# Kernel optimization log

Measured on AMD Instinct MI355X. Metric: run time of the kernel, lower is better.

## Reference

```python
import jax, jax.numpy as jnp
import numpy as np

DIM = 1024
NUM_HEADS = 16
HEAD_DIM = DIM // NUM_HEADS


def setup_inputs() -> dict:
    key = jax.random.key(0)
    k1, k2, k3, k4, k5 = jax.random.split(key, 5)
    scale = 0.02
    return {
        "x": jax.random.normal(k1, (4, 2048, DIM), dtype=jnp.float32),
        "w_qkv": jax.random.normal(k2, (DIM, 3 * DIM), dtype=jnp.float32) * scale,
        "b_qkv": jax.random.normal(k3, (3 * DIM,), dtype=jnp.float32) * scale,
        "w_proj": jax.random.normal(k4, (DIM, DIM), dtype=jnp.float32) * scale,
        "b_proj": jax.random.normal(k5, (DIM,), dtype=jnp.float32) * scale,
    }


def reference(x, w_qkv, b_qkv, w_proj, b_proj):
    B, N, C = x.shape
    H, D = NUM_HEADS, HEAD_DIM
    qkv = x @ w_qkv + b_qkv                      # [B, N, 3C]
    qkv = qkv.reshape(B, N, 3, H, D)
    q = qkv[:, :, 0].transpose(0, 2, 1, 3)       # [B, H, N, D]
    k = qkv[:, :, 1].transpose(0, 2, 1, 3)
    v = qkv[:, :, 2].transpose(0, 2, 1, 3)
    attn = jnp.einsum("bhnd,bhmd->bhnm", q, k) / (D ** 0.5)  # [B, H, N, N]
    attn = jax.nn.softmax(attn, axis=-1)
    out = jnp.einsum("bhnm,bhmd->bhnd", attn, v)  # [B, H, N, D]
    out = out.transpose(0, 2, 1, 3).reshape(B, N, C)
    return out @ w_proj + b_proj
```

## Files before the change

### kernel.cpp

```cpp
#include <hip/hip_runtime.h>
#include <stdint.h>

typedef __bf16 bf16_t;
typedef __bf16 bf16x8 __attribute__((ext_vector_type(8)));
typedef __bf16 bf16x4 __attribute__((ext_vector_type(4)));
typedef float  f32x4  __attribute__((ext_vector_type(4)));

__device__ __forceinline__ void g2l16(const void* g, void* l) {
    __builtin_amdgcn_global_load_lds(
        (const __attribute__((address_space(1))) unsigned int*)g,
        (__attribute__((address_space(3))) unsigned int*)l, 16, 0, 0);
}


__global__ __launch_bounds__(256) void cvt_bf16_kernel(
    const float* __restrict__ in, bf16_t* __restrict__ out, int n)
{
    int i = blockIdx.x * 256 + threadIdx.x;
    int idx = i * 4;
    if (idx >= n) return;
    const float4 v = *(const float4*)(in + idx);
    bf16x4 o;
    o[0] = (bf16_t)v.x; o[1] = (bf16_t)v.y; o[2] = (bf16_t)v.z; o[3] = (bf16_t)v.w;
    *(bf16x4*)(out + idx) = o;
}

__global__ __launch_bounds__(256) void tcvt_kernel(
    const float* __restrict__ in, bf16_t* __restrict__ out, int R, int C)
{
    __shared__ float t[32][33];
    const int c0 = blockIdx.x * 32, r0 = blockIdx.y * 32;
    const int x = threadIdx.x & 31, y = threadIdx.x >> 5;
    #pragma unroll
    for (int i = 0; i < 32; i += 8)
        t[y + i][x] = in[(size_t)(r0 + y + i) * C + c0 + x];
    __syncthreads();
    #pragma unroll
    for (int i = 0; i < 32; i += 8)
        out[(size_t)(c0 + y + i) * R + r0 + x] = (bf16_t)t[x][y + i];
}

__device__ __forceinline__ void gemm128(
    const bf16_t* __restrict__ A, const bf16_t* __restrict__ Bt, const int K,
    bf16_t* sA, bf16_t* sB, const int m0, const int n0, f32x4 acc[4][4])
{
    const int tid  = threadIdx.x;
    const int lane = tid & 63;
    const int w    = tid >> 6;
    const int wm   = (w >> 1) * 64;
    const int wn   = (w & 1) * 64;
    const int col0 = lane & 15;
    const int quad = lane >> 4;

    #pragma unroll
    for (int mt = 0; mt < 4; ++mt)
        #pragma unroll
        for (int nt = 0; nt < 4; ++nt)
            acc[mt][nt] = (f32x4){0.f, 0.f, 0.f, 0.f};

    const int srow = tid >> 3;
    const int jsw  = ((tid & 7) ^ (srow & 7)) << 3;
    const bf16_t* Ab = A  + (size_t)(m0 + srow) * K + jsw;
    const bf16_t* Bb = Bt + (size_t)(n0 + srow) * K + jsw;

    for (int kb = 0; kb < K; kb += 64) {
        #pragma unroll
        for (int it = 0; it < 4; ++it) {
            g2l16(Ab + (size_t)(it * 32) * K + kb, sA + (size_t)(it * 256 + tid) * 8);
            g2l16(Bb + (size_t)(it * 32) * K + kb, sB + (size_t)(it * 256 + tid) * 8);
        }
        __syncthreads();
        #pragma unroll
        for (int ks = 0; ks < 2; ++ks) {
            const int jg = ks * 4 + quad;
            bf16x8 af[4], bv[4];
            #pragma unroll
            for (int mt = 0; mt < 4; ++mt) {
                const int ra = wm + mt * 16 + col0;
                af[mt] = *(const bf16x8*)(sA + ra * 64 + ((jg ^ (ra & 7)) << 3));
            }
            #pragma unroll
            for (int nt = 0; nt < 4; ++nt) {
                const int rb = wn + nt * 16 + col0;
                bv[nt] = *(const bf16x8*)(sB + rb * 64 + ((jg ^ (rb & 7)) << 3));
            }
            #pragma unroll
            for (int mt = 0; mt < 4; ++mt)
                #pragma unroll
                for (int nt = 0; nt < 4; ++nt)
                    acc[mt][nt] = __builtin_amdgcn_mfma_f32_16x16x32_bf16(
                        af[mt], bv[nt], acc[mt][nt], 0, 0, 0);
        }
        __syncthreads();
    }
}

#define QSCALE 0.18033688f
__global__ __launch_bounds__(256) void qkv_gemm_kernel(
    const bf16_t* __restrict__ x, const bf16_t* __restrict__ wT,
    const float* __restrict__ bias,
    bf16_t* __restrict__ q, bf16_t* __restrict__ k, bf16_t* __restrict__ vT)
{
    __shared__ bf16_t sA[128 * 64];
    __shared__ bf16_t sB[128 * 64];
    const int m0 = blockIdx.y * 128;
    const int n0 = blockIdx.x * 128;
    f32x4 acc[4][4];
    gemm128(x, wT, 1024, sA, sB, m0, n0, acc);

    const int tid = threadIdx.x, lane = tid & 63, w = tid >> 6;
    const int wm = (w >> 1) * 64, wn = (w & 1) * 64;
    const int col0 = lane & 15, quad = lane >> 4;
    const int sel = n0 >> 10;

    #pragma unroll
    for (int mt = 0; mt < 4; ++mt) {
        const int m_base = m0 + wm + mt * 16 + quad * 4;
        const int b = m_base >> 11;
        const int t = m_base & 2047;
        #pragma unroll
        for (int nt = 0; nt < 4; ++nt) {
            const int n = n0 + wn + nt * 16 + col0;
            const float bvv = bias[n];
            const int h = (n >> 6) & 15, d = n & 63;
            const size_t bh = (size_t)b * 16 + h;
            if (sel == 0) {
                #pragma unroll
                for (int r = 0; r < 4; ++r)
                    q[(bh * 2048 + t + r) * 64 + d] = (bf16_t)((acc[mt][nt][r] + bvv) * QSCALE);
            } else if (sel == 1) {
                #pragma unroll
                for (int r = 0; r < 4; ++r)
                    k[(bh * 2048 + t + r) * 64 + d] = (bf16_t)(acc[mt][nt][r] + bvv);
            } else {
                #pragma unroll
                for (int r = 0; r < 4; ++r)
                    vT[(bh * 64 + d) * 2048 + t + r] = (bf16_t)(acc[mt][nt][r] + bvv);
            }
        }
    }
}

__global__ __launch_bounds__(256) void proj_gemm_kernel(
    const bf16_t* __restrict__ a, const bf16_t* __restrict__ wT,
    const float* __restrict__ bias, float* __restrict__ out)
{
    __shared__ bf16_t sA[128 * 64];
    __shared__ bf16_t sB[128 * 64];
    const int m0 = blockIdx.y * 128;
    const int n0 = blockIdx.x * 128;
    f32x4 acc[4][4];
    gemm128(a, wT, 1024, sA, sB, m0, n0, acc);

    const int tid = threadIdx.x, lane = tid & 63, w = tid >> 6;
    const int wm = (w >> 1) * 64, wn = (w & 1) * 64;
    const int col0 = lane & 15, quad = lane >> 4;
    #pragma unroll
    for (int mt = 0; mt < 4; ++mt) {
        const int m_base = m0 + wm + mt * 16 + quad * 4;
        #pragma unroll
        for (int nt = 0; nt < 4; ++nt) {
            const int n = n0 + wn + nt * 16 + col0;
            const float bvv = bias[n];
            #pragma unroll
            for (int r = 0; r < 4; ++r)
                out[(size_t)(m_base + r) * 1024 + n] = acc[mt][nt][r] + bvv;
        }
    }
}

#define SP_STRIDE 72
__global__ __launch_bounds__(256) void attn_kernel(
    const bf16_t* __restrict__ q, const bf16_t* __restrict__ k,
    const bf16_t* __restrict__ vT, bf16_t* __restrict__ out)
{
    __shared__ __align__(16) char smem[18432 + 16384 + 16384];
    bf16_t* sQ = (bf16_t*)smem;
    bf16_t* sP = (bf16_t*)smem;
    bf16_t* sK = (bf16_t*)(smem + 18432);
    bf16_t* sV = (bf16_t*)(smem + 18432 + 16384);

    const int bh = blockIdx.y;
    const int qb = blockIdx.x;
    const int tid = threadIdx.x, lane = tid & 63, w = tid >> 6;
    const int col0 = lane & 15, quad = lane >> 4;

    const bf16_t* qbase = q  + ((size_t)bh * 2048 + qb * 128) * 64;
    const bf16_t* kbase = k  + (size_t)bh * 2048 * 64;
    const bf16_t* vbase = vT + (size_t)bh * 64 * 2048;

    const int srow8  = tid >> 3;
    const int jsw8   = ((tid & 7) ^ (srow8 & 7)) << 3;
    const int srow16 = tid >> 4;
    const int jsw16  = ((tid & 15) ^ (srow16 & 15)) << 3;

    #pragma unroll
    for (int it = 0; it < 4; ++it)
        g2l16(qbase + (size_t)(it * 32 + srow8) * 64 + jsw8,
              sQ + (size_t)(it * 256 + tid) * 8);
    __syncthreads();

    bf16x8 qf[2][2];
    #pragma unroll
    for (int mt = 0; mt < 2; ++mt)
        #pragma unroll
        for (int ks = 0; ks < 2; ++ks) {
            const int rq = w * 32 + mt * 16 + col0;
            const int jg = ks * 4 + quad;
            qf[mt][ks] = *(const bf16x8*)(sQ + rq * 64 + ((jg ^ (rq & 7)) << 3));
        }

    f32x4 oacc[2][4];
    float row_l[2][4];
    #pragma unroll
    for (int mt = 0; mt < 2; ++mt) {
        #pragma unroll
        for (int nt = 0; nt < 4; ++nt) oacc[mt][nt] = (f32x4){0.f, 0.f, 0.f, 0.f};
        #pragma unroll
        for (int r = 0; r < 4; ++r) row_l[mt][r] = 0.f;
    }

    for (int kv = 0; kv < 16; ++kv) {
        __syncthreads();
        const bf16_t* kg = kbase + (size_t)kv * 128 * 64;
        #pragma unroll
        for (int it = 0; it < 4; ++it)
            g2l16(kg + (size_t)(it * 32 + srow8) * 64 + jsw8,
                  sK + (size_t)(it * 256 + tid) * 8);
        #pragma unroll
        for (int it = 0; it < 4; ++it) {
            const int d = it * 16 + srow16;
            g2l16(vbase + (size_t)d * 2048 + kv * 128 + jsw16,
                  sV + (size_t)(it * 256 + tid) * 8);
        }
        __syncthreads();

        f32x4 s[2][8];
        #pragma unroll
        for (int mt = 0; mt < 2; ++mt)
            #pragma unroll
            for (int nt = 0; nt < 8; ++nt) s[mt][nt] = (f32x4){0.f, 0.f, 0.f, 0.f};
        #pragma unroll
        for (int ks = 0; ks < 2; ++ks) {
            const int jg = ks * 4 + quad;
            bf16x8 kf[8];
            #pragma unroll
            for (int nt = 0; nt < 8; ++nt) {
                const int rk = nt * 16 + col0;
                kf[nt] = *(const bf16x8*)(sK + rk * 64 + ((jg ^ (rk & 7)) << 3));
            }
            #pragma unroll
            for (int mt = 0; mt < 2; ++mt)
                #pragma unroll
                for (int nt = 0; nt < 8; ++nt)
                    s[mt][nt] = __builtin_amdgcn_mfma_f32_16x16x32_bf16(
                        qf[mt][ks], kf[nt], s[mt][nt], 0, 0, 0);
        }

        #pragma unroll
        for (int mt = 0; mt < 2; ++mt)
            #pragma unroll
            for (int r = 0; r < 4; ++r) {
                float rs = 0.f;
                #pragma unroll
                for (int nt = 0; nt < 8; ++nt) {
                    const float p = __builtin_amdgcn_exp2f(s[mt][nt][r]);
                    s[mt][nt][r] = p;
                    rs += p;
                }
                row_l[mt][r] += rs;
            }

        #pragma unroll
        for (int half = 0; half < 2; ++half) {
            #pragma unroll
            for (int mt = 0; mt < 2; ++mt)
                #pragma unroll
                for (int nt = 0; nt < 4; ++nt)
                    #pragma unroll
                    for (int r = 0; r < 4; ++r)
                        sP[(w * 32 + mt * 16 + quad * 4 + r) * SP_STRIDE + nt * 16 + col0] =
                            (bf16_t)s[mt][half * 4 + nt][r];
            #pragma unroll
            for (int ks = 0; ks < 2; ++ks) {
                bf16x8 pf[2], vf[4];
                #pragma unroll
                for (int mt = 0; mt < 2; ++mt)
                    pf[mt] = *(const bf16x8*)(sP + (w * 32 + mt * 16 + col0) * SP_STRIDE
                                              + ks * 32 + quad * 8);
                #pragma unroll
                for (int nt = 0; nt < 4; ++nt) {
                    const int dv = nt * 16 + col0;
                    const int jg = half * 8 + ks * 4 + quad;
                    vf[nt] = *(const bf16x8*)(sV + dv * 128 + ((jg ^ (dv & 15)) << 3));
                }
                #pragma unroll
                for (int mt = 0; mt < 2; ++mt)
                    #pragma unroll
                    for (int nt = 0; nt < 4; ++nt)
                        oacc[mt][nt] = __builtin_amdgcn_mfma_f32_16x16x32_bf16(
                            pf[mt], vf[nt], oacc[mt][nt], 0, 0, 0);
            }
        }
    }

    const int b = bh >> 4, h = bh & 15;
    #pragma unroll
    for (int mt = 0; mt < 2; ++mt) {
        #pragma unroll
        for (int r = 0; r < 4; ++r) {
            float l = row_l[mt][r];
            #pragma unroll
            for (int off = 1; off < 16; off <<= 1) l += __shfl_xor(l, off);
            const float inv = 1.0f / l;
            const int t = qb * 128 + w * 32 + mt * 16 + quad * 4 + r;
            const size_t rowbase = ((size_t)b * 2048 + t) * 1024 + h * 64;
            #pragma unroll
            for (int nt = 0; nt < 4; ++nt)
                out[rowbase + nt * 16 + col0] = (bf16_t)(oacc[mt][nt][r] * inv);
        }
    }
}

extern "C" void kernel_launch(void* const* d_in, const int* in_sizes, int n_in,
                              void* d_out, int out_size, void* d_ws, size_t ws_size,
                              hipStream_t stream) {
    const float* x      = (const float*)d_in[0];
    const float* w_qkv  = (const float*)d_in[1];
    const float* b_qkv  = (const float*)d_in[2];
    const float* w_proj = (const float*)d_in[3];
    const float* b_proj = (const float*)d_in[4];
    float* out = (float*)d_out;

    char* p = (char*)d_ws;
    bf16_t* x_bf   = (bf16_t*)p; p += (size_t)8192 * 1024 * 2;
    bf16_t* wqkvT  = (bf16_t*)p; p += (size_t)3072 * 1024 * 2;
    bf16_t* wprojT = (bf16_t*)p; p += (size_t)1024 * 1024 * 2;
    bf16_t* qb     = (bf16_t*)p; p += (size_t)8192 * 1024 * 2;
    bf16_t* kb     = (bf16_t*)p; p += (size_t)8192 * 1024 * 2;
    bf16_t* vTb    = (bf16_t*)p; p += (size_t)8192 * 1024 * 2;
    bf16_t* attb   = (bf16_t*)p; p += (size_t)8192 * 1024 * 2;

    cvt_bf16_kernel<<<8192, 256, 0, stream>>>(x, x_bf, 8192 * 1024);
    tcvt_kernel<<<dim3(96, 32), 256, 0, stream>>>(w_qkv, wqkvT, 1024, 3072);
    tcvt_kernel<<<dim3(32, 32), 256, 0, stream>>>(w_proj, wprojT, 1024, 1024);
    qkv_gemm_kernel<<<dim3(24, 64), 256, 0, stream>>>(x_bf, wqkvT, b_qkv, qb, kb, vTb);
    attn_kernel<<<dim3(16, 64), 256, 0, stream>>>(qb, kb, vTb, attb);
    proj_gemm_kernel<<<dim3(8, 64), 256, 0, stream>>>(attb, wprojT, b_proj, out);
}
```

Before: 293.3 us.

## Process two query tiles per attention block to reuse loaded K/V tiles

```diff
diff --git a/kernel.cpp b/kernel.cpp
--- a/kernel.cpp
+++ b/kernel.cpp
@@ -174,18 +174,18 @@
     const bf16_t* __restrict__ q, const bf16_t* __restrict__ k,
     const bf16_t* __restrict__ vT, bf16_t* __restrict__ out)
 {
-    __shared__ __align__(16) char smem[18432 + 16384 + 16384];
+    __shared__ __align__(16) char smem[32768 + 16384 + 16384];
     bf16_t* sQ = (bf16_t*)smem;
     bf16_t* sP = (bf16_t*)smem;
-    bf16_t* sK = (bf16_t*)(smem + 18432);
-    bf16_t* sV = (bf16_t*)(smem + 18432 + 16384);
+    bf16_t* sK = (bf16_t*)(smem + 32768);
+    bf16_t* sV = (bf16_t*)(smem + 32768 + 16384);
 
     const int bh = blockIdx.y;
     const int qb = blockIdx.x;
     const int tid = threadIdx.x, lane = tid & 63, w = tid >> 6;
     const int col0 = lane & 15, quad = lane >> 4;
 
-    const bf16_t* qbase = q  + ((size_t)bh * 2048 + qb * 128) * 64;
+    const bf16_t* qbase = q  + ((size_t)bh * 2048 + qb * 256) * 64;
     const bf16_t* kbase = k  + (size_t)bh * 2048 * 64;
     const bf16_t* vbase = vT + (size_t)bh * 64 * 2048;
 
@@ -195,30 +195,34 @@
     const int jsw16  = ((tid & 15) ^ (srow16 & 15)) << 3;
 
     #pragma unroll
-    for (int it = 0; it < 4; ++it)
+    for (int it = 0; it < 8; ++it)
         g2l16(qbase + (size_t)(it * 32 + srow8) * 64 + jsw8,
               sQ + (size_t)(it * 256 + tid) * 8);
     __syncthreads();
 
-    bf16x8 qf[2][2];
-    #pragma unroll
-    for (int mt = 0; mt < 2; ++mt)
-        #pragma unroll
-        for (int ks = 0; ks < 2; ++ks) {
-            const int rq = w * 32 + mt * 16 + col0;
-            const int jg = ks * 4 + quad;
-            qf[mt][ks] = *(const bf16x8*)(sQ + rq * 64 + ((jg ^ (rq & 7)) << 3));
-        }
-
-    f32x4 oacc[2][4];
-    float row_l[2][4];
-    #pragma unroll
-    for (int mt = 0; mt < 2; ++mt) {
-        #pragma unroll
-        for (int nt = 0; nt < 4; ++nt) oacc[mt][nt] = (f32x4){0.f, 0.f, 0.f, 0.f};
-        #pragma unroll
-        for (int r = 0; r < 4; ++r) row_l[mt][r] = 0.f;
-    }
+    bf16x8 qf[2][2][2];
+    #pragma unroll
+    for (int qt = 0; qt < 2; ++qt)
+        #pragma unroll
+        for (int mt = 0; mt < 2; ++mt)
+            #pragma unroll
+            for (int ks = 0; ks < 2; ++ks) {
+                const int rq = qt * 128 + w * 32 + mt * 16 + col0;
+                const int jg = ks * 4 + quad;
+                qf[qt][mt][ks] = *(const bf16x8*)(sQ + rq * 64 + ((jg ^ (rq & 7)) << 3));
+            }
+
+    f32x4 oacc[2][2][4];
+    float row_l[2][2][4];
+    #pragma unroll
+    for (int qt = 0; qt < 2; ++qt)
+        #pragma unroll
+        for (int mt = 0; mt < 2; ++mt) {
+            #pragma unroll
+            for (int nt = 0; nt < 4; ++nt) oacc[qt][mt][nt] = (f32x4){0.f, 0.f, 0.f, 0.f};
+            #pragma unroll
+            for (int r = 0; r < 4; ++r) row_l[qt][mt][r] = 0.f;
+        }
 
     for (int kv = 0; kv < 16; ++kv) {
         __syncthreads();
@@ -235,91 +239,96 @@
         }
         __syncthreads();
 
-        f32x4 s[2][8];
-        #pragma unroll
-        for (int mt = 0; mt < 2; ++mt)
-            #pragma unroll
-            for (int nt = 0; nt < 8; ++nt) s[mt][nt] = (f32x4){0.f, 0.f, 0.f, 0.f};
-        #pragma unroll
-        for (int ks = 0; ks < 2; ++ks) {
-            const int jg = ks * 4 + quad;
-            bf16x8 kf[8];
-            #pragma unroll
-            for (int nt = 0; nt < 8; ++nt) {
-                const int rk = nt * 16 + col0;
-                kf[nt] = *(const bf16x8*)(sK + rk * 64 + ((jg ^ (rk & 7)) << 3));
-            }
+        #pragma unroll
+        for (int qt = 0; qt < 2; ++qt) {
+            f32x4 s[2][8];
             #pragma unroll
             for (int mt = 0; mt < 2; ++mt)
                 #pragma unroll
-                for (int nt = 0; nt < 8; ++nt)
-                    s[mt][nt] = __builtin_amdgcn_mfma_f32_16x16x32_bf16(
-                        qf[mt][ks], kf[nt], s[mt][nt], 0, 0, 0);
-        }
-
-        #pragma unroll
-        for (int mt = 0; mt < 2; ++mt)
+                for (int nt = 0; nt < 8; ++nt) s[mt][nt] = (f32x4){0.f, 0.f, 0.f, 0.f};
+            #pragma unroll
+            for (int ks = 0; ks < 2; ++ks) {
+                const int jg = ks * 4 + quad;
+                bf16x8 kf[8];
+                #pragma unroll
+                for (int nt = 0; nt < 8; ++nt) {
+                    const int rk = nt * 16 + col0;
+                    kf[nt] = *(const bf16x8*)(sK + rk * 64 + ((jg ^ (rk & 7)) << 3));
+                }
+                #pragma unroll
+                for (int mt = 0; mt < 2; ++mt)
+                    #pragma unroll
+                    for (int nt = 0; nt < 8; ++nt)
+                        s[mt][nt] = __builtin_amdgcn_mfma_f32_16x16x32_bf16(
+                            qf[qt][mt][ks], kf[nt], s[mt][nt], 0, 0, 0);
+            }
+
+            #pragma unroll
+            for (int mt = 0; mt < 2; ++mt)
+                #pragma unroll
+                for (int r = 0; r < 4; ++r) {
+                    float rs = 0.f;
+                    #pragma unroll
+                    for (int nt = 0; nt < 8; ++nt) {
+                        const float p = __builtin_amdgcn_exp2f(s[mt][nt][r]);
+                        s[mt][nt][r] = p;
+                        rs += p;
+                    }
+                    row_l[qt][mt][r] += rs;
+                }
+
+            #pragma unroll
+            for (int half = 0; half < 2; ++half) {
+                #pragma unroll
+                for (int mt = 0; mt < 2; ++mt)
+                    #pragma unroll
+                    for (int nt = 0; nt < 4; ++nt)
+                        #pragma unroll
+                        for (int r = 0; r < 4; ++r)
+                            sP[(w * 32 + mt * 16 + quad * 4 + r) * SP_STRIDE + nt * 16 + col0] =
+                                (bf16_t)s[mt][half * 4 + nt][r];
+                #pragma unroll
+                for (int ks = 0; ks < 2; ++ks) {
+                    bf16x8 pf[2], vf[4];
+                    #pragma unroll
+                    for (int mt = 0; mt < 2; ++mt)
+                        pf[mt] = *(const bf16x8*)(sP + (w * 32 + mt * 16 + col0) * SP_STRIDE
+                                                  + ks * 32 + quad * 8);
+                    #pragma unroll
+                    for (int nt = 0; nt < 4; ++nt) {
+                        const int dv = nt * 16 + col0;
+                        const int jg = half * 8 + ks * 4 + quad;
+                        vf[nt] = *(const bf16x8*)(sV + dv * 128 + ((jg ^ (dv & 15)) << 3));
+                    }
+                    #pragma unroll
+                    for (int mt = 0; mt < 2; ++mt)
+                        #pragma unroll
+                        for (int nt = 0; nt < 4; ++nt)
+                            oacc[qt][mt][nt] = __builtin_amdgcn_mfma_f32_16x16x32_bf16(
+                                pf[mt], vf[nt], oacc[qt][mt][nt], 0, 0, 0);
+                }
+            }
+        }
+    }
+
+    const int b = bh >> 4, h = bh & 15;
+    #pragma unroll
+    for (int qt = 0; qt < 2; ++qt)
+        #pragma unroll
+        for (int mt = 0; mt < 2; ++mt) {
             #pragma unroll
             for (int r = 0; r < 4; ++r) {
-                float rs = 0.f;
-                #pragma unroll
-                for (int nt = 0; nt < 8; ++nt) {
-                    const float p = __builtin_amdgcn_exp2f(s[mt][nt][r]);
-                    s[mt][nt][r] = p;
-                    rs += p;
-                }
-                row_l[mt][r] += rs;
-            }
-
-        #pragma unroll
-        for (int half = 0; half < 2; ++half) {
-            #pragma unroll
-            for (int mt = 0; mt < 2; ++mt)
+                float l = row_l[qt][mt][r];
+                #pragma unroll
+                for (int off = 1; off < 16; off <<= 1) l += __shfl_xor(l, off);
+                const float inv = 1.0f / l;
+                const int t = qb * 256 + qt * 128 + w * 32 + mt * 16 + quad * 4 + r;
+                const size_t rowbase = ((size_t)b * 2048 + t) * 1024 + h * 64;
                 #pragma unroll
                 for (int nt = 0; nt < 4; ++nt)
-                    #pragma unroll
-                    for (int r = 0; r < 4; ++r)
-                        sP[(w * 32 + mt * 16 + quad * 4 + r) * SP_STRIDE + nt * 16 + col0] =
-                            (bf16_t)s[mt][half * 4 + nt][r];
-            #pragma unroll
-            for (int ks = 0; ks < 2; ++ks) {
-                bf16x8 pf[2], vf[4];
-                #pragma unroll
-                for (int mt = 0; mt < 2; ++mt)
-                    pf[mt] = *(const bf16x8*)(sP + (w * 32 + mt * 16 + col0) * SP_STRIDE
-                                              + ks * 32 + quad * 8);
-                #pragma unroll
-                for (int nt = 0; nt < 4; ++nt) {
-                    const int dv = nt * 16 + col0;
-                    const int jg = half * 8 + ks * 4 + quad;
-                    vf[nt] = *(const bf16x8*)(sV + dv * 128 + ((jg ^ (dv & 15)) << 3));
-                }
-                #pragma unroll
-                for (int mt = 0; mt < 2; ++mt)
-                    #pragma unroll
-                    for (int nt = 0; nt < 4; ++nt)
-                        oacc[mt][nt] = __builtin_amdgcn_mfma_f32_16x16x32_bf16(
-                            pf[mt], vf[nt], oacc[mt][nt], 0, 0, 0);
-            }
-        }
-    }
-
-    const int b = bh >> 4, h = bh & 15;
-    #pragma unroll
-    for (int mt = 0; mt < 2; ++mt) {
-        #pragma unroll
-        for (int r = 0; r < 4; ++r) {
-            float l = row_l[mt][r];
-            #pragma unroll
-            for (int off = 1; off < 16; off <<= 1) l += __shfl_xor(l, off);
-            const float inv = 1.0f / l;
-            const int t = qb * 128 + w * 32 + mt * 16 + quad * 4 + r;
-            const size_t rowbase = ((size_t)b * 2048 + t) * 1024 + h * 64;
-            #pragma unroll
-            for (int nt = 0; nt < 4; ++nt)
-                out[rowbase + nt * 16 + col0] = (bf16_t)(oacc[mt][nt][r] * inv);
-        }
-    }
+                    out[rowbase + nt * 16 + col0] = (bf16_t)(oacc[qt][mt][r ? nt : nt][r] * inv);
+            }
+        }
 }
 
 extern "C" void kernel_launch(void* const* d_in, const int* in_sizes, int n_in,
@@ -345,6 +354,6 @@
     tcvt_kernel<<<dim3(96, 32), 256, 0, stream>>>(w_qkv, wqkvT, 1024, 3072);
     tcvt_kernel<<<dim3(32, 32), 256, 0, stream>>>(w_proj, wprojT, 1024, 1024);
     qkv_gemm_kernel<<<dim3(24, 64), 256, 0, stream>>>(x_bf, wqkvT, b_qkv, qb, kb, vTb);
-    attn_kernel<<<dim3(16, 64), 256, 0, stream>>>(qb, kb, vTb, attb);
+    attn_kernel<<<dim3(8, 64), 256, 0, stream>>>(qb, kb, vTb, attb);
     proj_gemm_kernel<<<dim3(8, 64), 256, 0, stream>>>(attb, wprojT, b_proj, out);
 }
```

New measurement: 327.5 us. 1.12x slower.
